# Kernel tuning notes

Hardware: AMD Instinct MI355X
Metric: run time of the kernel (lower is better)

## Reference

```python
import jax, jax.numpy as jnp
import numpy as np

B, T, D = 2, 2048, 2048
H, KVH = 32, 8
HD = D // H            # 64
G = H // KVH           # 4


def setup_inputs() -> dict:
    key = jax.random.key(0)
    k1, k2, k3 = jax.random.split(key, 3)
    x_q = jax.random.normal(k1, (B, T, D), dtype=jnp.float32)
    W_qkv = jax.random.normal(k2, (D, H * HD + 2 * KVH * HD), dtype=jnp.float32) * 0.02
    W_out = jax.random.normal(k3, (D, D), dtype=jnp.float32) * 0.02
    b_out = jnp.zeros((D,), dtype=jnp.float32)
    # real rotary tables: theta = 10000^{-2i/HD}
    inv_freq = 1.0 / (10000.0 ** (np.arange(0, HD, 2) / HD))   # [HD/2]
    pos = np.arange(T)[:, None] * inv_freq[None, :]            # [T, HD/2]
    rope_cos = jnp.asarray(np.cos(pos), dtype=jnp.float32)
    rope_sin = jnp.asarray(np.sin(pos), dtype=jnp.float32)
    return {"x_q": x_q, "W_qkv": W_qkv, "W_out": W_out, "b_out": b_out,
            "rope_cos": rope_cos, "rope_sin": rope_sin}


def _apply_rope(x, cos, sin):
    # x: [B, h, T, HD], cos/sin: [T, HD/2] -> interleaved even/odd rotation
    xe = x[..., 0::2]
    xo = x[..., 1::2]
    c = cos[None, None, :, :]
    s = sin[None, None, :, :]
    return jnp.stack([xe * c - xo * s, xe * s + xo * c], axis=-1).reshape(x.shape)


def reference(x_q, W_qkv, W_out, b_out, rope_cos, rope_sin):
    b, t, d = x_q.shape
    qkv = x_q @ W_qkv                                  # [B,T,3072]
    q_lin = qkv[..., : H * HD]
    k_lin = qkv[..., H * HD: H * HD + KVH * HD]
    v_lin = qkv[..., H * HD + KVH * HD:]
    q = q_lin.reshape(b, t, H, HD).transpose(0, 2, 1, 3)        # [B,H,T,HD]
    k = k_lin.reshape(b, t, KVH, HD).transpose(0, 2, 1, 3)      # [B,KVH,T,HD]
    v = v_lin.reshape(b, t, KVH, HD).transpose(0, 2, 1, 3)
    # GQA expand (repeat_interleave over heads)
    k = jnp.repeat(k, G, axis=1)                                # [B,H,T,HD]
    v = jnp.repeat(v, G, axis=1)
    q = _apply_rope(q, rope_cos[:t], rope_sin[:t])
    k = _apply_rope(k, rope_cos[:t], rope_sin[:t])
    scale = 1.0 / jnp.sqrt(jnp.asarray(HD, dtype=x_q.dtype))
    logits = jnp.einsum('bhqd,bhkd->bhqk', q, k) * scale        # [B,H,T,T]
    causal = jnp.triu(jnp.ones((t, t), dtype=bool), 1)[None, None]
    logits = jnp.where(causal, jnp.finfo(logits.dtype).min, logits)
    attn = jax.nn.softmax(logits, axis=-1)
    out = jnp.einsum('bhqk,bhkd->bhqd', attn, v)                # [B,H,T,HD]
    out = out.transpose(0, 2, 1, 3).reshape(b, t, H * HD)       # [B,T,D]
    out = out @ W_out + b_out
    return jnp.nan_to_num(out, nan=0.0, posinf=1e4, neginf=-1e4)
```

## Files before the change

### kernel.cpp

```cpp
#include <hip/hip_runtime.h>
#include <hip/hip_bf16.h>

#define DI __device__ __forceinline__

#if __has_builtin(__builtin_amdgcn_exp2f)
#define EXP2(x) __builtin_amdgcn_exp2f(x)
#else
#define EXP2(x) exp2f(x)
#endif

namespace {

constexpr int Bc = 2, Tc = 2048, Dc = 2048, Hc = 32, KVHc = 8, HDc = 64;
constexpr int NQKV = Hc * HDc + 2 * KVHc * HDc;

typedef __bf16 bf16x8 __attribute__((ext_vector_type(8)));
typedef unsigned short u16x8 __attribute__((ext_vector_type(8)));
typedef unsigned short u16x4 __attribute__((ext_vector_type(4)));
typedef float f32x4 __attribute__((ext_vector_type(4)));

union FragU { u16x8 u; bf16x8 b; u16x4 h[2]; };

DI float bits2f(unsigned int u) {
  union { unsigned int i; float f; } v; v.i = u << 16; return v.f;
}
DI unsigned short f2bits(float f) {
  __hip_bfloat16 h = __float2bfloat16(f);
  return *reinterpret_cast<unsigned short*>(&h);
}

DI void store_out(float* p, float v) { *p = v; }
DI void store_out(__hip_bfloat16* p, float v) { *p = __float2bfloat16(v); }

typedef __attribute__((address_space(1))) void gv_t;
typedef __attribute__((address_space(3))) void lv_t;

template<int ROWB, int TOTB, bool SWZ = false>
DI void stage_tile(const char* g, long long row_stride_b, char* lds) {
  const int tid = threadIdx.x;
  const int wid = tid >> 6, lane = tid & 63;
#pragma unroll
  for (int it = 0; it < TOTB / 4096; ++it) {
    int off = it * 4096 + wid * 1024 + lane * 16;
    int row = off / ROWB;
    int colb = off % ROWB;
    if (SWZ) colb ^= (row & 7) << 4;
    const char* gp = g + (long long)row * row_stride_b + colb;
    char* lp = lds + it * 4096 + wid * 1024;
    __builtin_amdgcn_global_load_lds((gv_t*)gp, (lv_t*)lp, 16, 0, 0);
  }
}

__global__ __launch_bounds__(256) void cvt_f32_bf16(
    const float* __restrict__ in, __hip_bfloat16* __restrict__ out) {
  const long long i = ((long long)blockIdx.x * 256 + threadIdx.x) * 8;
  const float4 a = *(const float4*)(in + i);
  const float4 b = *(const float4*)(in + i + 4);
  u16x8 r;
  r[0] = f2bits(a.x); r[1] = f2bits(a.y); r[2] = f2bits(a.z); r[3] = f2bits(a.w);
  r[4] = f2bits(b.x); r[5] = f2bits(b.y); r[6] = f2bits(b.z); r[7] = f2bits(b.w);
  *(u16x8*)((unsigned short*)out + i) = r;
}

__global__ __launch_bounds__(256) void transpose_cvt_kernel(
    const float* __restrict__ in, __hip_bfloat16* __restrict__ out, int R, int C) {
  __shared__ unsigned short tile[64][65];
  const int c0 = blockIdx.x * 64, r0 = blockIdx.y * 64;
  const int tid = threadIdx.x;
  const int rr = tid >> 2, seg = (tid & 3) * 16;
  const float* src = in + (long long)(r0 + rr) * C + c0 + seg;
#pragma unroll
  for (int i = 0; i < 16; ++i) tile[rr][seg + i] = f2bits(src[i]);
  __syncthreads();
  unsigned short* dst = (unsigned short*)out + (long long)(c0 + rr) * R + r0 + seg;
#pragma unroll
  for (int i = 0; i < 16; ++i) dst[i] = tile[seg + i][rr];
}

__global__ __launch_bounds__(256) void transpose_kernel(
    const __hip_bfloat16* __restrict__ in, __hip_bfloat16* __restrict__ out,
    int R, int C) {
  __shared__ unsigned short tile[64][65];
  const long long slice = (long long)R * C;
  const unsigned short* ip = (const unsigned short*)in + (long long)blockIdx.z * slice;
  unsigned short* op = (unsigned short*)out + (long long)blockIdx.z * slice;
  const int c0 = blockIdx.x * 64, r0 = blockIdx.y * 64;
  const int tid = threadIdx.x;
  const int rr = tid >> 2, seg = (tid & 3) * 16;
  const unsigned short* src = ip + (long long)(r0 + rr) * C + c0 + seg;
#pragma unroll
  for (int i = 0; i < 16; ++i) tile[rr][seg + i] = src[i];
  __syncthreads();
  unsigned short* dst = op + (long long)(c0 + rr) * R + r0 + seg;
#pragma unroll
  for (int i = 0; i < 16; ++i) dst[i] = tile[seg + i][rr];
}

template <typename OT>
__global__ __launch_bounds__(256) void gemm_bt(
    const __hip_bfloat16* __restrict__ A, const __hip_bfloat16* __restrict__ Bt,
    const float* __restrict__ bias, OT* __restrict__ C, int M, int N, int K) {
  __shared__ __align__(16) char As[8192];
  __shared__ __align__(16) char Bs[8192];
  const int n0 = blockIdx.x * 128;
  const int m0 = blockIdx.y * 128;
  const int tid = threadIdx.x;
  const int wid = tid >> 6, lane = tid & 63;
  const int wm = (wid >> 1) * 64, wn = (wid & 1) * 64;
  const int l15 = lane & 15, quad = lane >> 4;

  f32x4 acc[4][4] = {};

  const int nk = K >> 5;
  for (int kt = 0; kt < nk; ++kt) {
    __syncthreads();
    stage_tile<64, 8192>((const char*)(A + (long long)m0 * K + kt * 32), (long long)K * 2, As);
    stage_tile<64, 8192>((const char*)(Bt + (long long)n0 * K + kt * 32), (long long)K * 2, Bs);
    __syncthreads();

    FragU a[4], b[4];
#pragma unroll
    for (int mt = 0; mt < 4; ++mt)
      a[mt].u = *(const u16x8*)(As + ((wm + mt * 16 + l15) * 32 + quad * 8) * 2);
#pragma unroll
    for (int nt = 0; nt < 4; ++nt)
      b[nt].u = *(const u16x8*)(Bs + ((wn + nt * 16 + l15) * 32 + quad * 8) * 2);
#pragma unroll
    for (int mt = 0; mt < 4; ++mt)
#pragma unroll
      for (int nt = 0; nt < 4; ++nt)
        acc[mt][nt] = __builtin_amdgcn_mfma_f32_16x16x32_bf16(a[mt].b, b[nt].b, acc[mt][nt], 0, 0, 0);
  }

#pragma unroll
  for (int nt = 0; nt < 4; ++nt) {
    const int col = n0 + wn + nt * 16 + l15;
    const float bv = bias ? bias[col] : 0.f;
#pragma unroll
    for (int mt = 0; mt < 4; ++mt) {
#pragma unroll
      for (int r = 0; r < 4; ++r) {
        const int row = m0 + wm + mt * 16 + quad * 4 + r;
        store_out(C + (long long)row * N + col, acc[mt][nt][r] + bv);
      }
    }
  }
}

__global__ __launch_bounds__(384) void rope_reshape(
    const __hip_bfloat16* __restrict__ qkv, const float* __restrict__ cosb,
    const float* __restrict__ sinb, __hip_bfloat16* __restrict__ Qo,
    __hip_bfloat16* __restrict__ Ko, __hip_bfloat16* __restrict__ Vo) {
  constexpr float SCL = 0.125f * 1.44269504088896f;
  const int row = blockIdx.x;
  const int b = row / Tc, t = row % Tc;
  const unsigned short* src = (const unsigned short*)qkv + (long long)row * NQKV;
  const float* cb = cosb + t * 32;
  const float* sb = sinb + t * 32;
  const int e = (int)threadIdx.x * 8;
  const u16x8 v = *(const u16x8*)(src + e);
  if (e < Hc * HDc) {
    const int hh = e >> 6, d = e & 63, ii = d >> 1;
    u16x8 r;
#pragma unroll
    for (int p = 0; p < 4; ++p) {
      const float c = cb[ii + p], s = sb[ii + p];
      const float xe = bits2f(v[2 * p]), xo = bits2f(v[2 * p + 1]);
      r[2 * p] = f2bits((xe * c - xo * s) * SCL);
      r[2 * p + 1] = f2bits((xe * s + xo * c) * SCL);
    }
    const long long idx = (((long long)b * Hc + hh) * Tc + t) * HDc + d;
    *(u16x8*)((unsigned short*)Qo + idx) = r;
  } else if (e < Hc * HDc + KVHc * HDc) {
    const int e2 = e - Hc * HDc;
    const int kh = e2 >> 6, d = e2 & 63, ii = d >> 1;
    u16x8 r;
#pragma unroll
    for (int p = 0; p < 4; ++p) {
      const float c = cb[ii + p], s = sb[ii + p];
      const float xe = bits2f(v[2 * p]), xo = bits2f(v[2 * p + 1]);
      r[2 * p] = f2bits(xe * c - xo * s);
      r[2 * p + 1] = f2bits(xe * s + xo * c);
    }
    const long long idx = (((long long)b * KVHc + kh) * Tc + t) * HDc + d;
    *(u16x8*)((unsigned short*)Ko + idx) = r;
  } else {
    const int e2 = e - (Hc * HDc + KVHc * HDc);
    const int kh = e2 >> 6, d = e2 & 63;
    const long long idx = (((long long)b * KVHc + kh) * Tc + t) * HDc + d;
    *(u16x8*)((unsigned short*)Vo + idx) = v;
  }
}

DI void attn_tile(const char* __restrict__ Ksb, const char* __restrict__ Vsb,
                  const FragU (&qa)[2], f32x4 (&O)[4], float& m_i, float& l_i,
                  bool diag, int wid, int l15, int quad, int sw) {
  f32x4 S[4] = {};
#pragma unroll
  for (int nt = 0; nt < 4; ++nt) {
#pragma unroll
    for (int ks = 0; ks < 2; ++ks) {
      FragU kb;
      kb.u = *(const u16x8*)(Ksb + (nt * 16 + l15) * 128 + ((((ks << 2) | quad) ^ sw) << 4));
      S[nt] = __builtin_amdgcn_mfma_f32_16x16x32_bf16(kb.b, qa[ks].b, S[nt], 0, 0, 0);
    }
  }

  if (diag) {
#pragma unroll
    for (int nt = 0; nt < 4; ++nt)
#pragma unroll
      for (int r = 0; r < 4; ++r)
        if ((nt * 16 + quad * 4 + r) > (wid * 16 + l15)) S[nt][r] = -1e30f;
  }

  float mx = fmaxf(fmaxf(S[0][0], S[0][1]), fmaxf(S[0][2], S[0][3]));
#pragma unroll
  for (int nt = 1; nt < 4; ++nt)
    mx = fmaxf(mx, fmaxf(fmaxf(S[nt][0], S[nt][1]), fmaxf(S[nt][2], S[nt][3])));
  mx = fmaxf(mx, __shfl_xor(mx, 16, 64));
  mx = fmaxf(mx, __shfl_xor(mx, 32, 64));
  const float mnew = fmaxf(m_i, mx);
  const float alpha = EXP2(m_i - mnew);
  m_i = mnew;

  float pe[4][4];
  float sum = 0.f;
#pragma unroll
  for (int nt = 0; nt < 4; ++nt)
#pragma unroll
    for (int r = 0; r < 4; ++r) {
      const float p = EXP2(S[nt][r] - mnew);
      pe[nt][r] = p;
      sum += p;
    }
  sum += __shfl_xor(sum, 16, 64);
  sum += __shfl_xor(sum, 32, 64);
  l_i = l_i * alpha + sum;

  FragU pa[2];
#pragma unroll
  for (int ks = 0; ks < 2; ++ks)
#pragma unroll
    for (int r = 0; r < 4; ++r) {
      pa[ks].u[r] = f2bits(pe[2 * ks][r]);
      pa[ks].u[4 + r] = f2bits(pe[2 * ks + 1][r]);
    }
#pragma unroll
  for (int nt = 0; nt < 4; ++nt)
#pragma unroll
    for (int r = 0; r < 4; ++r) O[nt][r] *= alpha;

#pragma unroll
  for (int nt = 0; nt < 4; ++nt) {
    const char* vrow = Vsb + (nt * 16 + l15) * 128 + ((quad & 1) << 3);
    const int gq = quad >> 1;
#pragma unroll
    for (int ks = 0; ks < 2; ++ks) {
      FragU vb;
      vb.h[0] = *(const u16x4*)(vrow + (((ks * 4 + gq) ^ sw) << 4));
      vb.h[1] = *(const u16x4*)(vrow + (((ks * 4 + gq + 2) ^ sw) << 4));
      O[nt] = __builtin_amdgcn_mfma_f32_16x16x32_bf16(vb.b, pa[ks].b, O[nt], 0, 0, 0);
    }
  }
}

__global__ __launch_bounds__(256, 4) void attn_kernel(
    const __hip_bfloat16* __restrict__ Q, const __hip_bfloat16* __restrict__ K,
    const __hip_bfloat16* __restrict__ Vt, __hip_bfloat16* __restrict__ Out) {
  __shared__ __align__(16) char QsA[8192];
  __shared__ __align__(16) char QsB[8192];
  __shared__ __align__(16) char Ks[8192];
  __shared__ __align__(16) char Vs[8192];

  const int p = blockIdx.x;
  const int qtA = p, qtB = (Tc / 64 - 1) - p;
  const int h = blockIdx.y, b = blockIdx.z;
  const int kvh = h >> 2;
  const int tid = threadIdx.x, wid = tid >> 6, lane = tid & 63;
  const int l15 = lane & 15, quad = lane >> 4;
  const int sw = l15 & 7;

  const char* QgA = (const char*)(Q + (((long long)b * Hc + h) * Tc + qtA * 64) * HDc);
  const char* QgB = (const char*)(Q + (((long long)b * Hc + h) * Tc + qtB * 64) * HDc);
  const char* Kg = (const char*)(K + (((long long)b * KVHc + kvh) * Tc) * HDc);
  const char* Vg = (const char*)(Vt + (((long long)b * KVHc + kvh) * HDc) * Tc);

  stage_tile<128, 8192, true>(QgA, 128, QsA);
  stage_tile<128, 8192, true>(QgB, 128, QsB);
  __syncthreads();

  FragU qaA[2], qaB[2];
#pragma unroll
  for (int ks = 0; ks < 2; ++ks) {
    const int qoff = (wid * 16 + l15) * 128 + ((((ks << 2) | quad) ^ sw) << 4);
    qaA[ks].u = *(const u16x8*)(QsA + qoff);
    qaB[ks].u = *(const u16x8*)(QsB + qoff);
  }

  f32x4 OA[4] = {}, OB[4] = {};
  float mA = -1e30f, lA = 0.f, mB = -1e30f, lB = 0.f;

  for (int j = 0; j <= qtB; ++j) {
    __syncthreads();
    stage_tile<128, 8192, true>(Kg + (long long)j * 8192, 128, Ks);
    stage_tile<128, 8192, true>(Vg + (long long)j * 128, (long long)Tc * 2, Vs);
    __syncthreads();

    attn_tile(Ks, Vs, qaB, OB, mB, lB, j == qtB, wid, l15, quad, sw);
    if (j <= qtA)
      attn_tile(Ks, Vs, qaA, OA, mA, lA, j == qtA, wid, l15, quad, sw);
  }

  const float invA = 1.0f / lA, invB = 1.0f / lB;
  const int tA = qtA * 64 + wid * 16 + l15;
  const int tB = qtB * 64 + wid * 16 + l15;
  unsigned short* obA =
      (unsigned short*)Out + ((long long)b * Tc + tA) * Dc + h * 64 + quad * 4;
  unsigned short* obB =
      (unsigned short*)Out + ((long long)b * Tc + tB) * Dc + h * 64 + quad * 4;
#pragma unroll
  for (int nt = 0; nt < 4; ++nt) {
    u16x4 va, vb;
#pragma unroll
    for (int r = 0; r < 4; ++r) {
      va[r] = f2bits(OA[nt][r] * invA);
      vb[r] = f2bits(OB[nt][r] * invB);
    }
    *(u16x4*)(obA + nt * 16) = va;
    *(u16x4*)(obB + nt * 16) = vb;
  }
}

}

extern "C" void kernel_launch(void* const* d_in, const int* in_sizes, int n_in,
                              void* d_out, int out_size, void* d_ws, size_t ws_size,
                              hipStream_t stream) {
  const float* x_q  = (const float*)d_in[0];
  const float* Wqkv = (const float*)d_in[1];
  const float* Wout = (const float*)d_in[2];
  const float* bout = (const float*)d_in[3];
  const float* rc   = (const float*)d_in[4];
  const float* rs   = (const float*)d_in[5];
  float* out = (float*)d_out;

  constexpr size_t SZ_QKV   = (size_t)Bc * Tc * NQKV * 2;
  constexpr size_t SZ_XB    = (size_t)Bc * Tc * Dc * 2;
  constexpr size_t SZ_QB    = (size_t)Bc * Hc * Tc * HDc * 2;
  constexpr size_t SZ_KV    = (size_t)Bc * KVHc * Tc * HDc * 2;
  constexpr size_t SZ_AO    = (size_t)Bc * Tc * Dc * 2;
  constexpr size_t OFF_QKV   = 0;
  constexpr size_t OFF_XB    = SZ_QKV;
  constexpr size_t OFF_WQKVT = SZ_QKV + SZ_XB;
  constexpr size_t OFF_QB    = SZ_QKV;
  constexpr size_t OFF_KB    = OFF_QB + SZ_QB;
  constexpr size_t OFF_VTMP  = OFF_KB + SZ_KV;
  constexpr size_t OFF_VT    = 0;
  constexpr size_t OFF_AO    = SZ_KV;
  constexpr size_t OFF_WOUTT = OFF_AO + SZ_AO;

  char* w = (char*)d_ws;
  __hip_bfloat16* qkv   = (__hip_bfloat16*)(w + OFF_QKV);
  __hip_bfloat16* xb    = (__hip_bfloat16*)(w + OFF_XB);
  __hip_bfloat16* WqkvT = (__hip_bfloat16*)(w + OFF_WQKVT);
  __hip_bfloat16* Qb    = (__hip_bfloat16*)(w + OFF_QB);
  __hip_bfloat16* Kb    = (__hip_bfloat16*)(w + OFF_KB);
  __hip_bfloat16* Vtmp  = (__hip_bfloat16*)(w + OFF_VTMP);
  __hip_bfloat16* Vt    = (__hip_bfloat16*)(w + OFF_VT);
  __hip_bfloat16* AO    = (__hip_bfloat16*)(w + OFF_AO);
  __hip_bfloat16* WoutT = (__hip_bfloat16*)(w + OFF_WOUTT);

  cvt_f32_bf16<<<dim3((Bc * Tc * Dc) / (256 * 8)), 256, 0, stream>>>(x_q, xb);

  transpose_cvt_kernel<<<dim3(NQKV / 64, Dc / 64), 256, 0, stream>>>(Wqkv, WqkvT, Dc, NQKV);

  gemm_bt<__hip_bfloat16><<<dim3(NQKV / 128, (Bc * Tc) / 128), 256, 0, stream>>>(
      xb, WqkvT, nullptr, qkv, Bc * Tc, NQKV, Dc);

  rope_reshape<<<dim3(Bc * Tc), 384, 0, stream>>>(qkv, rc, rs, Qb, Kb, Vtmp);

  transpose_kernel<<<dim3(HDc / 64, Tc / 64, Bc * KVHc), 256, 0, stream>>>(Vtmp, Vt, Tc, HDc);

  attn_kernel<<<dim3(Tc / 128, Hc, Bc), 256, 0, stream>>>(Qb, Kb, Vt, AO);

  transpose_cvt_kernel<<<dim3(Dc / 64, Dc / 64), 256, 0, stream>>>(Wout, WoutT, Dc, Dc);

  gemm_bt<float><<<dim3(Dc / 128, (Bc * Tc) / 128), 256, 0, stream>>>(
      AO, WoutT, bout, out, Bc * Tc, Dc, Dc);
}
```

Baseline: 374.0 us.

## Double-buffer K/V tiles in LDS and load Q fragments directly from global

Splits the K and V shared-memory tiles into two buffers so the next tile's global loads are issued before computing on the current one, overlapping memory latency with MFMA work and dropping one barrier per iteration. Q fragments are now read straight from global memory into registers, removing the Q staging buffers and keeping total LDS the same. The stage_tile path likely uses async global-to-LDS loads, hence the explicit vmcnt waits. Risks are uncoalesced Q reads and a full vmcnt drain each iteration limiting overlap.

```diff
diff --git a/kernel.cpp b/kernel.cpp
--- a/kernel.cpp
+++ b/kernel.cpp
@@ -268,10 +268,8 @@
 __global__ __launch_bounds__(256, 4) void attn_kernel(
     const __hip_bfloat16* __restrict__ Q, const __hip_bfloat16* __restrict__ K,
     const __hip_bfloat16* __restrict__ Vt, __hip_bfloat16* __restrict__ Out) {
-  __shared__ __align__(16) char QsA[8192];
-  __shared__ __align__(16) char QsB[8192];
-  __shared__ __align__(16) char Ks[8192];
-  __shared__ __align__(16) char Vs[8192];
+  __shared__ __align__(16) char Ks[2][8192];
+  __shared__ __align__(16) char Vs[2][8192];
 
   const int p = blockIdx.x;
   const int qtA = p, qtB = (Tc / 64 - 1) - p;
@@ -286,30 +284,35 @@
   const char* Kg = (const char*)(K + (((long long)b * KVHc + kvh) * Tc) * HDc);
   const char* Vg = (const char*)(Vt + (((long long)b * KVHc + kvh) * HDc) * Tc);
 
-  stage_tile<128, 8192, true>(QgA, 128, QsA);
-  stage_tile<128, 8192, true>(QgB, 128, QsB);
-  __syncthreads();
-
   FragU qaA[2], qaB[2];
 #pragma unroll
   for (int ks = 0; ks < 2; ++ks) {
-    const int qoff = (wid * 16 + l15) * 128 + ((((ks << 2) | quad) ^ sw) << 4);
-    qaA[ks].u = *(const u16x8*)(QsA + qoff);
-    qaB[ks].u = *(const u16x8*)(QsB + qoff);
+    const int qoff = (wid * 16 + l15) * 128 + (((ks << 2) | quad) << 4);
+    qaA[ks].u = *(const u16x8*)(QgA + qoff);
+    qaB[ks].u = *(const u16x8*)(QgB + qoff);
   }
 
   f32x4 OA[4] = {}, OB[4] = {};
   float mA = -1e30f, lA = 0.f, mB = -1e30f, lB = 0.f;
 
+  stage_tile<128, 8192, true>(Kg, 128, Ks[0]);
+  stage_tile<128, 8192, true>(Vg, (long long)Tc * 2, Vs[0]);
+  asm volatile("s_waitcnt vmcnt(0)" ::: "memory");
+  __syncthreads();
+
   for (int j = 0; j <= qtB; ++j) {
+    const int cur = j & 1;
+    if (j < qtB) {
+      stage_tile<128, 8192, true>(Kg + (long long)(j + 1) * 8192, 128, Ks[cur ^ 1]);
+      stage_tile<128, 8192, true>(Vg + (long long)(j + 1) * 128, (long long)Tc * 2, Vs[cur ^ 1]);
+    }
+
+    attn_tile(Ks[cur], Vs[cur], qaB, OB, mB, lB, j == qtB, wid, l15, quad, sw);
+    if (j <= qtA)
+      attn_tile(Ks[cur], Vs[cur], qaA, OA, mA, lA, j == qtA, wid, l15, quad, sw);
+
+    asm volatile("s_waitcnt vmcnt(0)" ::: "memory");
     __syncthreads();
-    stage_tile<128, 8192, true>(Kg + (long long)j * 8192, 128, Ks);
-    stage_tile<128, 8192, true>(Vg + (long long)j * 128, (long long)Tc * 2, Vs);
-    __syncthreads();
-
-    attn_tile(Ks, Vs, qaB, OB, mB, lB, j == qtB, wid, l15, quad, sw);
-    if (j <= qtA)
-      attn_tile(Ks, Vs, qaA, OA, mA, lA, j == qtA, wid, l15, quad, sw);
   }
 
   const float invA = 1.0f / lA, invB = 1.0f / lB;
```

Result: no change. 375.7 us (+0.5%).
